# Kernel optimization log

Measured on AMD Instinct MI355X. Metric: run time of the kernel, lower is better.

## Reference

```python
import jax, jax.numpy as jnp
import numpy as np

B, T, D = 2, 2048, 1024
E, K, FF = 8, 2, 4096


def setup_inputs() -> dict:
    key = jax.random.key(0)
    ks = jax.random.split(key, 4)
    scale = 0.02
    return {
        "x": jax.random.normal(ks[0], (B, T, D), jnp.float32),
        "gate_w": jax.random.normal(ks[1], (D, E), jnp.float32) * scale,
        "gate_b": jnp.zeros((E,), jnp.float32),
        "w1": jax.random.normal(ks[2], (E, D, FF), jnp.float32) * scale,
        "b1": jnp.zeros((E, FF), jnp.float32),
        "w2": jax.random.normal(ks[3], (E, FF, D), jnp.float32) * scale,
        "b2": jnp.zeros((E, D), jnp.float32),
    }


def reference(x, gate_w, gate_b, w1, b1, w2, b2):
    # x: (B,T,D). Original runs every expert densely over all tokens then masks;
    # since mask*x == x at selected positions and output is re-masked, the math
    # equals: output[t] = sum_k softmax(topk_vals)[k] * expert_{idx_k}(x)[t].
    n_experts = w1.shape[0]
    gate_logits = x @ gate_w + gate_b                      # (B,T,E)
    topk_vals, topk_idx = jax.lax.top_k(gate_logits, K)    # (B,T,K)
    topk_w = jax.nn.softmax(topk_vals, axis=-1)            # (B,T,K)
    onehot = jax.nn.one_hot(topk_idx, n_experts, dtype=x.dtype)  # (B,T,K,E)
    comb = jnp.sum(onehot * topk_w[..., None], axis=2)     # (B,T,E) combine weights

    # Dense per-expert FFN over all tokens (faithful to original redundant compute)
    h = jax.nn.gelu(jnp.einsum('btd,edf->ebtf', x, w1) + b1[:, None, None, :],
                    approximate=False)                      # (E,B,T,FF)
    y = jnp.einsum('ebtf,efd->ebtd', h, w2) + b2[:, None, None, :]  # (E,B,T,D)
    output = jnp.einsum('ebtd,bte->btd', y, comb)           # (B,T,D)

    expert_counts = jnp.sum(onehot, axis=(0, 1, 2)).astype(jnp.float32)  # (E,)
    return output, gate_logits, topk_idx, expert_counts
```

## Files before the change

### kernel.cpp

```cpp
#include <hip/hip_runtime.h>
#include <math.h>

#define NTOK 4096
#define DIM  1024
#define NE   8
#define FF   4096

#define OUT_LOGITS 4194304
#define OUT_IDX    4227072
#define OUT_CNT    4235264

typedef unsigned short u16;
typedef __bf16 bf16x8 __attribute__((ext_vector_type(8)));
typedef float  f32x4  __attribute__((ext_vector_type(4)));

__device__ __forceinline__ u16 f2bf(float f) {
  union { float f; unsigned u; } v; v.f = f;
  unsigned r = v.u + 0x7fffu + ((v.u >> 16) & 1u);
  return (u16)(r >> 16);
}

__device__ __forceinline__ void gload_lds16(const u16* g, u16* l) {
  __builtin_amdgcn_global_load_lds(
      (const __attribute__((address_space(1))) void*)(g),
      (__attribute__((address_space(3))) void*)(l), 16, 0, 0);
}

__global__ __launch_bounds__(256) void convert_x_kernel(const float* __restrict__ in,
                                                        u16* __restrict__ out) {
  int i = (blockIdx.x * 256 + threadIdx.x) * 4;
  float4 v = *(const float4*)(in + i);
  unsigned a = (unsigned)f2bf(v.x) | ((unsigned)f2bf(v.y) << 16);
  unsigned b = (unsigned)f2bf(v.z) | ((unsigned)f2bf(v.w) << 16);
  *(uint2*)(out + i) = make_uint2(a, b);
}

__global__ __launch_bounds__(256) void transpose_cvt_kernel(const float* __restrict__ in,
                                                            u16* __restrict__ out,
                                                            int R, int C) {
  __shared__ float tile[32][33];
  int ez = blockIdx.z;
  in  += (size_t)ez * R * C;
  out += (size_t)ez * R * C;
  int c0 = blockIdx.x * 32, r0 = blockIdx.y * 32;
  int tx = threadIdx.x, ty = threadIdx.y;
  #pragma unroll
  for (int j = ty; j < 32; j += 8)
    tile[j][tx] = in[(size_t)(r0 + j) * C + c0 + tx];
  __syncthreads();
  #pragma unroll
  for (int j = ty; j < 32; j += 8)
    out[(size_t)(c0 + j) * R + r0 + tx] = f2bf(tile[tx][j]);
}

__global__ __launch_bounds__(256) void gate_kernel(const float* __restrict__ x,
                                                   const float* __restrict__ gw,
                                                   const float* __restrict__ gb,
                                                   float* __restrict__ out,
                                                   int* __restrict__ counts,
                                                   int* __restrict__ tok_list,
                                                   float* __restrict__ wt_list) {
  int wave = threadIdx.x >> 6, lane = threadIdx.x & 63;
  int token = blockIdx.x * 4 + wave;
  const float* xr = x + (size_t)token * DIM + lane * 16;
  float acc[NE];
  #pragma unroll
  for (int e = 0; e < NE; e++) acc[e] = 0.f;
  #pragma unroll
  for (int c = 0; c < 16; c += 4) {
    float4 xv = *(const float4*)(xr + c);
    const float* gwr = gw + (size_t)(lane * 16 + c) * NE;
    float xs[4] = {xv.x, xv.y, xv.z, xv.w};
    #pragma unroll
    for (int q = 0; q < 4; q++)
      #pragma unroll
      for (int e = 0; e < NE; e++)
        acc[e] += xs[q] * gwr[q * NE + e];
  }
  #pragma unroll
  for (int off = 32; off; off >>= 1)
    #pragma unroll
    for (int e = 0; e < NE; e++)
      acc[e] += __shfl_down(acc[e], off);

  if (lane == 0) {
    float lg[NE];
    #pragma unroll
    for (int e = 0; e < NE; e++) {
      lg[e] = acc[e] + gb[e];
      out[OUT_LOGITS + token * NE + e] = lg[e];
    }
    int i0 = 0; float v0 = lg[0];
    #pragma unroll
    for (int e = 1; e < NE; e++) if (lg[e] > v0) { v0 = lg[e]; i0 = e; }
    int i1 = -1; float v1 = -1e30f;
    #pragma unroll
    for (int e = 0; e < NE; e++) if (e != i0 && lg[e] > v1) { v1 = lg[e]; i1 = e; }
    float ex = expf(v1 - v0);
    float s = 1.f + ex;
    float w0 = 1.f / s, w1 = ex / s;
    out[OUT_IDX + token * 2]     = (float)i0;
    out[OUT_IDX + token * 2 + 1] = (float)i1;
    int s0 = atomicAdd(&counts[i0], 1);
    tok_list[i0 * NTOK + s0] = token; wt_list[i0 * NTOK + s0] = w0;
    int s1 = atomicAdd(&counts[i1], 1);
    tok_list[i1 * NTOK + s1] = token; wt_list[i1 * NTOK + s1] = w1;
  }
}

__global__ void scan_kernel(const int* __restrict__ counts, int* __restrict__ offsets,
                            float* __restrict__ cnt_out) {
  if (threadIdx.x == 0) {
    int off = 0;
    for (int e = 0; e < NE; e++) { offsets[e] = off; off += counts[e]; }
  }
  if (threadIdx.x < NE) cnt_out[threadIdx.x] = (float)counts[threadIdx.x];
}

template <int MODE>
__global__ __launch_bounds__(256) void moe_gemm_kernel(
    const u16* __restrict__ Abase, const u16* __restrict__ Bbase,
    const float* __restrict__ bias,
    const int* __restrict__ counts, const int* __restrict__ offsets,
    const int* __restrict__ tok_list, const float* __restrict__ wt_list,
    u16* __restrict__ Hout, float* __restrict__ Out) {
  constexpr int KT = (MODE == 0) ? DIM : FF;
  constexpr int NT = (MODE == 0) ? FF : DIM;
  const int e  = blockIdx.z;
  const int ne = counts[e];
  const int m0 = blockIdx.y * 128;
  if (m0 >= ne) return;
  const int n0   = blockIdx.x * 128;
  const int offs = offsets[e];

  __shared__ u16 As[128 * 32];
  __shared__ u16 Bs[128 * 32];

  const int t = threadIdx.x;
  const int wave = t >> 6, lane = t & 63;
  const int quad = lane >> 4, l16 = lane & 15;
  const int wm = (wave & 1) * 64, wn = (wave >> 1) * 64;

  const int colA = (t & 3) * 8;
  const u16* aptr[2];
  const u16* bptr[2];
  #pragma unroll
  for (int p = 0; p < 2; p++) {
    int s  = m0 + p * 64 + (t >> 2);
    int sr = s < ne ? s : ne - 1;
    size_t arow;
    if (MODE == 0) arow = (size_t)tok_list[e * NTOK + sr] * (size_t)KT;
    else           arow = (size_t)(offs + sr) * (size_t)KT;
    aptr[p] = Abase + arow + colA;
    bptr[p] = Bbase + (size_t)e * NT * KT + (size_t)(n0 + p * 64 + (t >> 2)) * KT + colA;
  }
  u16* asDst[2] = { &As[t * 8], &As[2048 + t * 8] };
  u16* bsDst[2] = { &Bs[t * 8], &Bs[2048 + t * 8] };

  f32x4 acc[4][4];
  #pragma unroll
  for (int i = 0; i < 4; i++)
    #pragma unroll
    for (int j = 0; j < 4; j++)
      acc[i][j] = (f32x4){0.f, 0.f, 0.f, 0.f};

  for (int k0 = 0; k0 < KT; k0 += 32) {
    gload_lds16(aptr[0] + k0, asDst[0]);
    gload_lds16(aptr[1] + k0, asDst[1]);
    gload_lds16(bptr[0] + k0, bsDst[0]);
    gload_lds16(bptr[1] + k0, bsDst[1]);
    __syncthreads();
    bf16x8 af[4], bfr[4];
    #pragma unroll
    for (int i = 0; i < 4; i++) {
      af[i]  = *(const bf16x8*)&As[(wm + i * 16 + l16) * 32 + quad * 8];
      bfr[i] = *(const bf16x8*)&Bs[(wn + i * 16 + l16) * 32 + quad * 8];
    }
    #pragma unroll
    for (int i = 0; i < 4; i++)
      #pragma unroll
      for (int j = 0; j < 4; j++)
        acc[i][j] = __builtin_amdgcn_mfma_f32_16x16x32_bf16(af[i], bfr[j], acc[i][j], 0, 0, 0);
    __syncthreads();
  }

  if (MODE == 0) {
    const float* bb = bias + (size_t)e * FF + n0;
    #pragma unroll
    for (int i = 0; i < 4; i++) {
      #pragma unroll
      for (int r = 0; r < 4; r++) {
        int s = m0 + wm + i * 16 + quad * 4 + r;
        if (s < ne) {
          u16* hr = Hout + (size_t)(offs + s) * FF + n0;
          #pragma unroll
          for (int j = 0; j < 4; j++) {
            int nl = wn + j * 16 + l16;
            float v = acc[i][j][r] + bb[nl];
            v = 0.5f * v * (1.f + erff(v * 0.70710678118654752f));
            hr[nl] = f2bf(v);
          }
        }
      }
    }
  } else {
    const float* bb = bias + (size_t)e * DIM + n0;
    #pragma unroll
    for (int i = 0; i < 4; i++) {
      #pragma unroll
      for (int r = 0; r < 4; r++) {
        int s = m0 + wm + i * 16 + quad * 4 + r;
        if (s < ne) {
          int   tok = tok_list[e * NTOK + s];
          float w   = wt_list[e * NTOK + s];
          float* orow = Out + (size_t)tok * DIM + n0;
          #pragma unroll
          for (int j = 0; j < 4; j++) {
            int nl = wn + j * 16 + l16;
            float v = (acc[i][j][r] + bb[nl]) * w;
            atomicAdd(&orow[nl], v);
          }
        }
      }
    }
  }
}

extern "C" void kernel_launch(void* const* d_in, const int* in_sizes, int n_in,
                              void* d_out, int out_size, void* d_ws, size_t ws_size,
                              hipStream_t stream) {
  const float* x   = (const float*)d_in[0];
  const float* gw  = (const float*)d_in[1];
  const float* gb  = (const float*)d_in[2];
  const float* w1  = (const float*)d_in[3];
  const float* b1  = (const float*)d_in[4];
  const float* w2  = (const float*)d_in[5];
  const float* b2  = (const float*)d_in[6];
  float* out = (float*)d_out;
  char*  ws  = (char*)d_ws;

  u16* x_bf  = (u16*)(ws);
  u16* w1t   = (u16*)(ws + 8388608);
  u16* w2t   = (u16*)(ws + 8388608 + 67108864);
  u16* h     = (u16*)(ws + 8388608 + 2ull * 67108864);
  char* meta = ws + 8388608 + 3ull * 67108864;
  int*   counts   = (int*)(meta);
  int*   offsets  = (int*)(meta + 32);
  int*   tok_list = (int*)(meta + 64);
  float* wt_list  = (float*)(meta + 64 + NE * NTOK * 4);
  (void)in_sizes; (void)n_in; (void)out_size; (void)ws_size;

  hipMemsetAsync(out, 0, (size_t)OUT_LOGITS * 4, stream);
  hipMemsetAsync(counts, 0, 32, stream);

  convert_x_kernel<<<NTOK * DIM / (256 * 4), 256, 0, stream>>>(x, x_bf);
  transpose_cvt_kernel<<<dim3(FF / 32, DIM / 32, NE), dim3(32, 8), 0, stream>>>(w1, w1t, DIM, FF);
  transpose_cvt_kernel<<<dim3(DIM / 32, FF / 32, NE), dim3(32, 8), 0, stream>>>(w2, w2t, FF, DIM);
  gate_kernel<<<NTOK / 4, 256, 0, stream>>>(x, gw, gb, out, counts, tok_list, wt_list);
  scan_kernel<<<1, 64, 0, stream>>>(counts, offsets, out + OUT_CNT);
  moe_gemm_kernel<0><<<dim3(FF / 128, NTOK / 128, NE), 256, 0, stream>>>(
      x_bf, w1t, b1, counts, offsets, tok_list, wt_list, h, nullptr);
  moe_gemm_kernel<1><<<dim3(DIM / 128, NTOK / 128, NE), 256, 0, stream>>>(
      h, w2t, b2, counts, offsets, tok_list, wt_list, nullptr, out);
}
```

Before: 752.3 us.

## Vectorize transpose stores, swizzle LDS tiles, and split-K the second MoE GEMM

The transpose kernel now writes four packed bf16 values per thread as a ushort4 store instead of scalar 16-bit stores. The GEMM applies an XOR swizzle to the LDS column chunk on both the global-to-LDS load and the fragment reads, to reduce bank conflicts. The second GEMM splits K into two halves across a doubled grid, with only the first half adding bias, to raise parallelism when few blocks are active. The cost is twice the atomic adds on the output and more partial-sum traffic.

```diff
diff --git a/kernel.cpp b/kernel.cpp
--- a/kernel.cpp
+++ b/kernel.cpp
@@ -43,14 +43,19 @@
   in  += (size_t)ez * R * C;
   out += (size_t)ez * R * C;
   int c0 = blockIdx.x * 32, r0 = blockIdx.y * 32;
-  int tx = threadIdx.x, ty = threadIdx.y;
+  int t  = threadIdx.x;
+  int tx = t & 31, ty = t >> 5;
   #pragma unroll
   for (int j = ty; j < 32; j += 8)
     tile[j][tx] = in[(size_t)(r0 + j) * C + c0 + tx];
   __syncthreads();
-  #pragma unroll
-  for (int j = ty; j < 32; j += 8)
-    out[(size_t)(c0 + j) * R + r0 + tx] = f2bf(tile[tx][j]);
+  int cc = t >> 3, rr0 = (t & 7) * 4;
+  ushort4 o;
+  o.x = f2bf(tile[rr0 + 0][cc]);
+  o.y = f2bf(tile[rr0 + 1][cc]);
+  o.z = f2bf(tile[rr0 + 2][cc]);
+  o.w = f2bf(tile[rr0 + 3][cc]);
+  *(ushort4*)(out + (size_t)(c0 + cc) * R + r0 + rr0) = o;
 }
 
 __global__ __launch_bounds__(256) void gate_kernel(const float* __restrict__ x,
@@ -130,7 +135,14 @@
   const int ne = counts[e];
   const int m0 = blockIdx.y * 128;
   if (m0 >= ne) return;
-  const int n0   = blockIdx.x * 128;
+  int n0, kbeg, kend;
+  if (MODE == 0) {
+    n0 = blockIdx.x * 128; kbeg = 0; kend = KT;
+  } else {
+    n0 = (blockIdx.x & 7) * 128;
+    int kc = blockIdx.x >> 3;
+    kbeg = kc * (KT / 2); kend = kbeg + KT / 2;
+  }
   const int offs = offsets[e];
 
   __shared__ u16 As[128 * 32];
@@ -141,7 +153,7 @@
   const int quad = lane >> 4, l16 = lane & 15;
   const int wm = (wave & 1) * 64, wn = (wave >> 1) * 64;
 
-  const int colA = (t & 3) * 8;
+  const int colA = ((t & 3) ^ ((t >> 3) & 3)) * 8;
   const u16* aptr[2];
   const u16* bptr[2];
   #pragma unroll
@@ -157,6 +169,8 @@
   u16* asDst[2] = { &As[t * 8], &As[2048 + t * 8] };
   u16* bsDst[2] = { &Bs[t * 8], &Bs[2048 + t * 8] };
 
+  const int swz = (l16 >> 1) & 3;
+
   f32x4 acc[4][4];
   #pragma unroll
   for (int i = 0; i < 4; i++)
@@ -164,17 +178,18 @@
     for (int j = 0; j < 4; j++)
       acc[i][j] = (f32x4){0.f, 0.f, 0.f, 0.f};
 
-  for (int k0 = 0; k0 < KT; k0 += 32) {
+  for (int k0 = kbeg; k0 < kend; k0 += 32) {
     gload_lds16(aptr[0] + k0, asDst[0]);
     gload_lds16(aptr[1] + k0, asDst[1]);
     gload_lds16(bptr[0] + k0, bsDst[0]);
     gload_lds16(bptr[1] + k0, bsDst[1]);
     __syncthreads();
     bf16x8 af[4], bfr[4];
+    const int cread = (quad ^ swz) * 8;
     #pragma unroll
     for (int i = 0; i < 4; i++) {
-      af[i]  = *(const bf16x8*)&As[(wm + i * 16 + l16) * 32 + quad * 8];
-      bfr[i] = *(const bf16x8*)&Bs[(wn + i * 16 + l16) * 32 + quad * 8];
+      af[i]  = *(const bf16x8*)&As[(wm + i * 16 + l16) * 32 + cread];
+      bfr[i] = *(const bf16x8*)&Bs[(wn + i * 16 + l16) * 32 + cread];
     }
     #pragma unroll
     for (int i = 0; i < 4; i++)
@@ -204,6 +219,7 @@
       }
     }
   } else {
+    const bool addb = (kbeg == 0);
     const float* bb = bias + (size_t)e * DIM + n0;
     #pragma unroll
     for (int i = 0; i < 4; i++) {
@@ -217,7 +233,7 @@
           #pragma unroll
           for (int j = 0; j < 4; j++) {
             int nl = wn + j * 16 + l16;
-            float v = (acc[i][j][r] + bb[nl]) * w;
+            float v = (acc[i][j][r] + (addb ? bb[nl] : 0.f)) * w;
             atomicAdd(&orow[nl], v);
           }
         }
@@ -254,12 +270,12 @@
   hipMemsetAsync(counts, 0, 32, stream);
 
   convert_x_kernel<<<NTOK * DIM / (256 * 4), 256, 0, stream>>>(x, x_bf);
-  transpose_cvt_kernel<<<dim3(FF / 32, DIM / 32, NE), dim3(32, 8), 0, stream>>>(w1, w1t, DIM, FF);
-  transpose_cvt_kernel<<<dim3(DIM / 32, FF / 32, NE), dim3(32, 8), 0, stream>>>(w2, w2t, FF, DIM);
+  transpose_cvt_kernel<<<dim3(FF / 32, DIM / 32, NE), 256, 0, stream>>>(w1, w1t, DIM, FF);
+  transpose_cvt_kernel<<<dim3(DIM / 32, FF / 32, NE), 256, 0, stream>>>(w2, w2t, FF, DIM);
   gate_kernel<<<NTOK / 4, 256, 0, stream>>>(x, gw, gb, out, counts, tok_list, wt_list);
   scan_kernel<<<1, 64, 0, stream>>>(counts, offsets, out + OUT_CNT);
   moe_gemm_kernel<0><<<dim3(FF / 128, NTOK / 128, NE), 256, 0, stream>>>(
       x_bf, w1t, b1, counts, offsets, tok_list, wt_list, h, nullptr);
-  moe_gemm_kernel<1><<<dim3(DIM / 128, NTOK / 128, NE), 256, 0, stream>>>(
+  moe_gemm_kernel<1><<<dim3(2 * DIM / 128, NTOK / 128, NE), 256, 0, stream>>>(
       h, w2t, b2, counts, offsets, tok_list, wt_list, nullptr, out);
 }
```

Result: slower. 767.9 us (+2.1%).

## Widen weight transpose tiles, build deterministic expert lists, pre-gather tokens, tanh GELU

Applied to the files above, without the earlier changes.

The weight transpose now uses 64x64 tiles with float4 loads and ushort4 stores, which cuts memory transactions in the large per-call fp32-to-bf16 weight conversion. Atomic token-list building is replaced by a single-block ballot/popcount pass that writes compact, deterministic per-expert lists and offsets. A gather kernel converts only the routed tokens into a contiguous bf16 buffer, so the first GEMM reads rows contiguously instead of indirectly. The exact erf GELU is swapped for a tanh approximation, which is cheaper but changes numerics slightly.

```diff
diff --git a/kernel.cpp b/kernel.cpp
--- a/kernel.cpp
+++ b/kernel.cpp
@@ -20,46 +20,54 @@
   return (u16)(r >> 16);
 }
 
+__device__ __forceinline__ float gelu_f(float v) {
+  float u = v * (0.7978845608f + 0.0356774081f * v * v);
+  float e = __expf(2.f * u);
+  float t = 1.f - 2.f / (e + 1.f);
+  return 0.5f * v * (1.f + t);
+}
+
 __device__ __forceinline__ void gload_lds16(const u16* g, u16* l) {
   __builtin_amdgcn_global_load_lds(
       (const __attribute__((address_space(1))) void*)(g),
       (__attribute__((address_space(3))) void*)(l), 16, 0, 0);
 }
 
-__global__ __launch_bounds__(256) void convert_x_kernel(const float* __restrict__ in,
-                                                        u16* __restrict__ out) {
-  int i = (blockIdx.x * 256 + threadIdx.x) * 4;
-  float4 v = *(const float4*)(in + i);
-  unsigned a = (unsigned)f2bf(v.x) | ((unsigned)f2bf(v.y) << 16);
-  unsigned b = (unsigned)f2bf(v.z) | ((unsigned)f2bf(v.w) << 16);
-  *(uint2*)(out + i) = make_uint2(a, b);
-}
-
 __global__ __launch_bounds__(256) void transpose_cvt_kernel(const float* __restrict__ in,
                                                             u16* __restrict__ out,
                                                             int R, int C) {
-  __shared__ float tile[32][33];
-  int ez = blockIdx.z;
-  in  += (size_t)ez * R * C;
-  out += (size_t)ez * R * C;
-  int c0 = blockIdx.x * 32, r0 = blockIdx.y * 32;
-  int tx = threadIdx.x, ty = threadIdx.y;
-  #pragma unroll
-  for (int j = ty; j < 32; j += 8)
-    tile[j][tx] = in[(size_t)(r0 + j) * C + c0 + tx];
+  __shared__ float tile[64][68];
+  in  += (size_t)blockIdx.z * R * C;
+  out += (size_t)blockIdx.z * R * C;
+  int c0 = blockIdx.x * 64, r0 = blockIdx.y * 64;
+  int t = threadIdx.x;
+  int cr = (t & 15) * 4, rr = t >> 4;
+  #pragma unroll
+  for (int p = 0; p < 4; p++) {
+    float4 v = *(const float4*)(in + (size_t)(r0 + rr + p * 16) * C + c0 + cr);
+    *(float4*)&tile[rr + p * 16][cr] = v;
+  }
   __syncthreads();
-  #pragma unroll
-  for (int j = ty; j < 32; j += 8)
-    out[(size_t)(c0 + j) * R + r0 + tx] = f2bf(tile[tx][j]);
+  int c = t >> 2, rb = (t & 3) * 4;
+  u16* orow = out + (size_t)(c0 + c) * R + r0;
+  #pragma unroll
+  for (int it = 0; it < 4; it++) {
+    int r = it * 16 + rb;
+    ushort4 o;
+    o.x = f2bf(tile[r + 0][c]);
+    o.y = f2bf(tile[r + 1][c]);
+    o.z = f2bf(tile[r + 2][c]);
+    o.w = f2bf(tile[r + 3][c]);
+    *(ushort4*)(orow + r) = o;
+  }
 }
 
 __global__ __launch_bounds__(256) void gate_kernel(const float* __restrict__ x,
                                                    const float* __restrict__ gw,
                                                    const float* __restrict__ gb,
                                                    float* __restrict__ out,
-                                                   int* __restrict__ counts,
-                                                   int* __restrict__ tok_list,
-                                                   float* __restrict__ wt_list) {
+                                                   int2* __restrict__ tk_idx,
+                                                   float2* __restrict__ tk_w) {
   int wave = threadIdx.x >> 6, lane = threadIdx.x & 63;
   int token = blockIdx.x * 4 + wave;
   const float* xr = x + (size_t)token * DIM + lane * 16;
@@ -98,23 +106,61 @@
     for (int e = 0; e < NE; e++) if (e != i0 && lg[e] > v1) { v1 = lg[e]; i1 = e; }
     float ex = expf(v1 - v0);
     float s = 1.f + ex;
-    float w0 = 1.f / s, w1 = ex / s;
     out[OUT_IDX + token * 2]     = (float)i0;
     out[OUT_IDX + token * 2 + 1] = (float)i1;
-    int s0 = atomicAdd(&counts[i0], 1);
-    tok_list[i0 * NTOK + s0] = token; wt_list[i0 * NTOK + s0] = w0;
-    int s1 = atomicAdd(&counts[i1], 1);
-    tok_list[i1 * NTOK + s1] = token; wt_list[i1 * NTOK + s1] = w1;
-  }
-}
-
-__global__ void scan_kernel(const int* __restrict__ counts, int* __restrict__ offsets,
-                            float* __restrict__ cnt_out) {
-  if (threadIdx.x == 0) {
-    int off = 0;
-    for (int e = 0; e < NE; e++) { offsets[e] = off; off += counts[e]; }
-  }
-  if (threadIdx.x < NE) cnt_out[threadIdx.x] = (float)counts[threadIdx.x];
+    tk_idx[token] = make_int2(i0, i1);
+    tk_w[token]   = make_float2(1.f / s, ex / s);
+  }
+}
+
+__global__ __launch_bounds__(512) void build_lists_kernel(
+    const int2* __restrict__ tk_idx, const float2* __restrict__ tk_w,
+    int* __restrict__ counts, int* __restrict__ offsets,
+    int* __restrict__ tok_list, float* __restrict__ wt_list,
+    float* __restrict__ cnt_out) {
+  __shared__ int s_cnt[NE];
+  int e = threadIdx.x >> 6, lane = threadIdx.x & 63;
+  int cnt = 0;
+  for (int base = 0; base < NTOK; base += 64) {
+    int2 idx = tk_idx[base + lane];
+    cnt += __popcll(__ballot(idx.x == e || idx.y == e));
+  }
+  if (lane == 0) s_cnt[e] = cnt;
+  __syncthreads();
+  int off = 0;
+  for (int ee = 0; ee < e; ee++) off += s_cnt[ee];
+  if (lane == 0) {
+    counts[e]  = s_cnt[e];
+    offsets[e] = off;
+    cnt_out[e] = (float)s_cnt[e];
+  }
+  int pos = off;
+  for (int base = 0; base < NTOK; base += 64) {
+    int tok = base + lane;
+    int2 idx = tk_idx[tok];
+    float2 w = tk_w[tok];
+    bool m0 = (idx.x == e), m1 = (idx.y == e);
+    bool m = m0 || m1;
+    unsigned long long mask = __ballot(m);
+    if (m) {
+      int p = pos + __popcll(mask & ((1ull << lane) - 1ull));
+      tok_list[p] = tok;
+      wt_list[p]  = m0 ? w.x : w.y;
+    }
+    pos += __popcll(mask);
+  }
+}
+
+__global__ __launch_bounds__(256) void gather_x_kernel(const float* __restrict__ x,
+                                                       const int* __restrict__ tok_list,
+                                                       u16* __restrict__ xg) {
+  int g = blockIdx.x;
+  int tok = tok_list[g];
+  int c = threadIdx.x * 4;
+  float4 v = *(const float4*)(x + (size_t)tok * DIM + c);
+  ushort4 o;
+  o.x = f2bf(v.x); o.y = f2bf(v.y); o.z = f2bf(v.z); o.w = f2bf(v.w);
+  *(ushort4*)(xg + (size_t)g * DIM + c) = o;
 }
 
 template <int MODE>
@@ -148,10 +194,7 @@
   for (int p = 0; p < 2; p++) {
     int s  = m0 + p * 64 + (t >> 2);
     int sr = s < ne ? s : ne - 1;
-    size_t arow;
-    if (MODE == 0) arow = (size_t)tok_list[e * NTOK + sr] * (size_t)KT;
-    else           arow = (size_t)(offs + sr) * (size_t)KT;
-    aptr[p] = Abase + arow + colA;
+    aptr[p] = Abase + (size_t)(offs + sr) * KT + colA;
     bptr[p] = Bbase + (size_t)e * NT * KT + (size_t)(n0 + p * 64 + (t >> 2)) * KT + colA;
   }
   u16* asDst[2] = { &As[t * 8], &As[2048 + t * 8] };
@@ -196,9 +239,7 @@
           #pragma unroll
           for (int j = 0; j < 4; j++) {
             int nl = wn + j * 16 + l16;
-            float v = acc[i][j][r] + bb[nl];
-            v = 0.5f * v * (1.f + erff(v * 0.70710678118654752f));
-            hr[nl] = f2bf(v);
+            hr[nl] = f2bf(gelu_f(acc[i][j][r] + bb[nl]));
           }
         }
       }
@@ -211,14 +252,13 @@
       for (int r = 0; r < 4; r++) {
         int s = m0 + wm + i * 16 + quad * 4 + r;
         if (s < ne) {
-          int   tok = tok_list[e * NTOK + s];
-          float w   = wt_list[e * NTOK + s];
+          int   tok = tok_list[offs + s];
+          float w   = wt_list[offs + s];
           float* orow = Out + (size_t)tok * DIM + n0;
           #pragma unroll
           for (int j = 0; j < 4; j++) {
             int nl = wn + j * 16 + l16;
-            float v = (acc[i][j][r] + bb[nl]) * w;
-            atomicAdd(&orow[nl], v);
+            atomicAdd(&orow[nl], (acc[i][j][r] + bb[nl]) * w);
           }
         }
       }
@@ -239,27 +279,29 @@
   float* out = (float*)d_out;
   char*  ws  = (char*)d_ws;
 
-  u16* x_bf  = (u16*)(ws);
-  u16* w1t   = (u16*)(ws + 8388608);
-  u16* w2t   = (u16*)(ws + 8388608 + 67108864);
-  u16* h     = (u16*)(ws + 8388608 + 2ull * 67108864);
-  char* meta = ws + 8388608 + 3ull * 67108864;
-  int*   counts   = (int*)(meta);
-  int*   offsets  = (int*)(meta + 32);
-  int*   tok_list = (int*)(meta + 64);
-  float* wt_list  = (float*)(meta + 64 + NE * NTOK * 4);
+  u16* w1t = (u16*)(ws);
+  u16* w2t = (u16*)(ws + 1ull * 67108864);
+  u16* h   = (u16*)(ws + 2ull * 67108864);
+  u16* xg  = (u16*)(ws + 3ull * 67108864);
+  char* meta = ws + 3ull * 67108864 + 16777216;
+  int*    counts   = (int*)(meta);
+  int*    offsets  = (int*)(meta + 64);
+  int*    tok_list = (int*)(meta + 128);
+  float*  wt_list  = (float*)(meta + 128 + 32768);
+  int2*   tk_idx   = (int2*)(meta + 128 + 2 * 32768);
+  float2* tk_w     = (float2*)(meta + 128 + 2 * 32768 + 32768);
   (void)in_sizes; (void)n_in; (void)out_size; (void)ws_size;
 
   hipMemsetAsync(out, 0, (size_t)OUT_LOGITS * 4, stream);
-  hipMemsetAsync(counts, 0, 32, stream);
-
-  convert_x_kernel<<<NTOK * DIM / (256 * 4), 256, 0, stream>>>(x, x_bf);
-  transpose_cvt_kernel<<<dim3(FF / 32, DIM / 32, NE), dim3(32, 8), 0, stream>>>(w1, w1t, DIM, FF);
-  transpose_cvt_kernel<<<dim3(DIM / 32, FF / 32, NE), dim3(32, 8), 0, stream>>>(w2, w2t, FF, DIM);
-  gate_kernel<<<NTOK / 4, 256, 0, stream>>>(x, gw, gb, out, counts, tok_list, wt_list);
-  scan_kernel<<<1, 64, 0, stream>>>(counts, offsets, out + OUT_CNT);
+
+  transpose_cvt_kernel<<<dim3(FF / 64, DIM / 64, NE), 256, 0, stream>>>(w1, w1t, DIM, FF);
+  transpose_cvt_kernel<<<dim3(DIM / 64, FF / 64, NE), 256, 0, stream>>>(w2, w2t, FF, DIM);
+  gate_kernel<<<NTOK / 4, 256, 0, stream>>>(x, gw, gb, out, tk_idx, tk_w);
+  build_lists_kernel<<<1, 512, 0, stream>>>(tk_idx, tk_w, counts, offsets, tok_list, wt_list,
+                                            out + OUT_CNT);
+  gather_x_kernel<<<2 * NTOK, 256, 0, stream>>>(x, tok_list, xg);
   moe_gemm_kernel<0><<<dim3(FF / 128, NTOK / 128, NE), 256, 0, stream>>>(
-      x_bf, w1t, b1, counts, offsets, tok_list, wt_list, h, nullptr);
+      xg, w1t, b1, counts, offsets, tok_list, wt_list, h, nullptr);
   moe_gemm_kernel<1><<<dim3(DIM / 128, NTOK / 128, NE), 256, 0, stream>>>(
       h, w2t, b2, counts, offsets, tok_list, wt_list, nullptr, out);
 }
```

Result: faster. 661.4 us (-12.1%).
